# Performance work log

Hardware: AMD Instinct MI355X
Metric: run time of the kernel (lower is better)

Reference implementation:

```python
import jax, jax.numpy as jnp
import numpy as np

NL, ND, NM = 16384, 4096, 2048   # LncRNA / Disease / MiRNA node counts
E = 262144                       # edges per relation
FEAT, HID, OUTF = 256, 64, 128
ITEMS, SIZE = 4096, 2048


def setup_inputs() -> dict:
    key = jax.random.key(0)
    ks = jax.random.split(key, 32)
    f32 = jnp.float32

    def ed(i, n_src, n_dst):
        return (jax.random.randint(ks[i], (E,), 0, n_src),
                jax.random.randint(ks[i + 1], (E,), 0, n_dst))

    src_LD, dst_LD = ed(0, NL, ND)
    src_DL, dst_DL = ed(2, ND, NL)
    src_LM, dst_LM = ed(4, NL, NM)
    src_ML, dst_ML = ed(6, NM, NL)
    src_DM, dst_DM = ed(8, ND, NM)
    src_MD, dst_MD = ed(10, NM, ND)

    inp = dict(
        h_L=jax.random.normal(ks[12], (NL, FEAT), f32),
        h_D=jax.random.normal(ks[13], (ND, FEAT), f32),
        h_M=jax.random.normal(ks[14], (NM, FEAT), f32),
        Adj=jax.random.uniform(ks[15], (SIZE, ITEMS), f32),
        src_LD=src_LD, dst_LD=dst_LD, src_DL=src_DL, dst_DL=dst_DL,
        src_LM=src_LM, dst_LM=dst_LM, src_ML=src_ML, dst_ML=dst_ML,
        src_DM=src_DM, dst_DM=dst_DM, src_MD=src_MD, dst_MD=dst_MD,
        # GraphConv weights, stacked over the 6 relations in order
        # [LvsD, DvsL, LvsM, MvsL, DvsM, MvsD]
        W1=jax.random.normal(ks[16], (6, FEAT, HID), f32) * 0.05,
        b1=jnp.zeros((6, HID), f32),
        W2=jax.random.normal(ks[17], (6, HID, HID), f32) * 0.05,
        b2=jnp.zeros((6, HID), f32),
        W3=jax.random.normal(ks[18], (6, HID, OUTF), f32) * 0.05,
        b3=jnp.zeros((6, OUTF), f32),
        # dense MLP head
        f1_w=jax.random.normal(ks[19], (ITEMS + OUTF, 256), f32) * 0.02,
        f1_b=jnp.zeros((256,), f32),
        f2_w=jax.random.normal(ks[20], (256, 512), f32) * 0.05,
        f2_b=jnp.zeros((512,), f32),
        f3_w=jax.random.normal(ks[21], (512, 1024), f32) * 0.05,
        f3_b=jnp.zeros((1024,), f32),
        f4_w=jax.random.normal(ks[22], (1024, ITEMS), f32) * 0.03,
        f4_b=jnp.zeros((ITEMS,), f32),
        size=SIZE,
        leftIndex=0,
    )
    return inp


def _gconv(x, src, dst, n_dst, W, b):
    """DGL GraphConv with norm='both': D_dst^{-1/2} A D_src^{-1/2} X W + b.
    Degrees are clamped to >=1 (DGL behavior)."""
    n_src = x.shape[0]
    ones = jnp.ones(src.shape[0], x.dtype)
    out_deg = jnp.clip(jax.ops.segment_sum(ones, src, num_segments=n_src), 1.0)
    in_deg = jnp.clip(jax.ops.segment_sum(ones, dst, num_segments=n_dst), 1.0)
    feat = x * jax.lax.rsqrt(out_deg)[:, None]
    m = jax.ops.segment_sum(feat[src], dst, num_segments=n_dst)
    m = m * jax.lax.rsqrt(in_deg)[:, None]
    return m @ W + b


def reference(h_L, h_D, h_M, Adj,
              W1, b1, W2, b2, W3, b3,
              f1_w, f1_b, f2_w, f2_b, f3_w, f3_b, f4_w, f4_b,
              src_LD, dst_LD, src_DL, dst_DL, src_LM, dst_LM,
              src_ML, dst_ML, src_DM, dst_DM, src_MD, dst_MD,
              size, leftIndex):

    def hetero_layer(hL, hD, hM, W, b):
        # aggregate='sum' over edge types per destination node type
        oD = (_gconv(hL, src_LD, dst_LD, ND, W[0], b[0])
              + _gconv(hM, src_MD, dst_MD, ND, W[5], b[5]))
        oL = (_gconv(hD, src_DL, dst_DL, NL, W[1], b[1])
              + _gconv(hM, src_ML, dst_ML, NL, W[3], b[3]))
        oM = (_gconv(hL, src_LM, dst_LM, NM, W[2], b[2])
              + _gconv(hD, src_DM, dst_DM, NM, W[4], b[4]))
        return oL, oD, oM

    hL, hD, hM = hetero_layer(h_L, h_D, h_M, W1, b1)
    hL, hD, hM = hetero_layer(hL, hD, hM, W2, b2)
    hL, hD, hM = hetero_layer(hL, hD, hM, W3, b3)

    # F.normalize(p=1, dim=1): x / max(||x||_1, 1e-12)
    l1 = jnp.maximum(jnp.sum(jnp.abs(hL), axis=1, keepdims=True), 1e-12)
    lncrna = hL / l1

    fake_embedding = lncrna[leftIndex:leftIndex + size]  # [size, OUTF]
    x = jnp.concatenate([Adj, fake_embedding], axis=1)   # [size, ITEMS+OUTF]
    x = jax.nn.relu(x @ f1_w + f1_b)
    x = jax.nn.relu(x @ f2_w + f2_b)
    x = jax.nn.relu(x @ f3_w + f3_b)
    x = jax.nn.sigmoid(x @ f4_w + f4_b)
    return (fake_embedding, x)
```

## Files before the change

### kernel.cpp

```cpp
#include <hip/hip_runtime.h>

constexpr int kNL = 16384, kND = 4096, kNM = 2048;
constexpr int kE = 262144;
constexpr int kFEAT = 256, kHID = 64, kOUTF = 128;
constexpr int kITEMS = 4096, kSIZE = 2048;
constexpr int kHB = 16;
constexpr int kZS = 128;
constexpr int kXIN = kITEMS + kOUTF;

typedef unsigned short ushort_t;
typedef unsigned int uint_t;
typedef __attribute__((ext_vector_type(8))) short short8v;
typedef __attribute__((ext_vector_type(4))) float f32x4;
typedef __attribute__((ext_vector_type(4))) uint_t uint4v;
typedef __attribute__((ext_vector_type(2))) uint_t uint2v;
typedef __attribute__((ext_vector_type(4))) int int4v;

struct EdgePtrs { const int* p[12]; };
struct I6 { int v[6]; };

__device__ inline ushort_t f2bf(float f) {
  unsigned u = __builtin_bit_cast(unsigned, f);
  unsigned r = u + 0x7fffu + ((u >> 16) & 1u);
  return (ushort_t)(r >> 16);
}
__device__ inline float bf2f(ushort_t b) {
  unsigned u = ((unsigned)b) << 16;
  return __builtin_bit_cast(float, u);
}
__device__ inline float bf2f_lo(uint_t v) { return __builtin_bit_cast(float, v << 16); }
__device__ inline float bf2f_hi(uint_t v) { return __builtin_bit_cast(float, v & 0xffff0000u); }

__device__ __forceinline__ void gload16(const ushort_t* g, ushort_t* l) {
  __builtin_amdgcn_global_load_lds(
      (const __attribute__((address_space(1))) void*)g,
      (__attribute__((address_space(3))) void*)l, 16, 0, 0);
}

__device__ __forceinline__ void xcd_swizzle(int& bx, int& by) {
  int gx = gridDim.x, gy = gridDim.y;
  int nwg = gx * gy;
  int orig = by * gx + bx;
  int q = nwg >> 3, r = nwg & 7;
  int xcd = orig & 7, loc = orig >> 3;
  int s = ((xcd < r) ? xcd * (q + 1) : r * (q + 1) + (xcd - r) * q) + loc;
  by = s % gy;
  bx = s / gy;
}

__global__ __launch_bounds__(256) void hist_kernel(EdgePtrs ep, uint_t* __restrict__ part) {
  __shared__ uint_t bins[16384];
  int k = blockIdx.x >> 4, chunk = blockIdx.x & (kHB - 1);
  uint4v zero = {0, 0, 0, 0};
  for (int i = threadIdx.x; i < 4096; i += 256) ((uint4v*)bins)[i] = zero;
  __syncthreads();
  const int4v* arr = (const int4v*)(ep.p[k] + chunk * (kE / kHB));
  for (int i = threadIdx.x; i < kE / kHB / 4; i += 256) {
    int4v e4 = arr[i];
    atomicAdd(&bins[e4[0]], 1u);
    atomicAdd(&bins[e4[1]], 1u);
    atomicAdd(&bins[e4[2]], 1u);
    atomicAdd(&bins[e4[3]], 1u);
  }
  __syncthreads();
  uint4v* o = (uint4v*)(part + ((size_t)blockIdx.x << 14));
  for (int i = threadIdx.x; i < 4096; i += 256) o[i] = ((uint4v*)bins)[i];
}

struct PJob { const float* in; ushort_t* out; int A; int B; int C; int kind; int nblk; };
struct PJobs { PJob j[24]; int n; };

__global__ __launch_bounds__(256) void prep_kernel(PJobs jobs) {
  __shared__ float t64[64][65];
  int b = blockIdx.x;
  int ji = 0;
  while (ji < jobs.n && b >= jobs.j[ji].nblk) { b -= jobs.j[ji].nblk; ++ji; }
  if (ji >= jobs.n) return;
  PJob jb = jobs.j[ji];
  if (jb.kind == 0) {
    int idx = b * 256 + threadIdx.x;
    if (idx >= jb.A) return;
    float4 v = ((const float4*)jb.in)[idx];
    uint2v pk;
    pk[0] = (uint_t)f2bf(v.x) | ((uint_t)f2bf(v.y) << 16);
    pk[1] = (uint_t)f2bf(v.z) | ((uint_t)f2bf(v.w) << 16);
    *(uint2v*)(jb.out + (size_t)idx * 4) = pk;
  } else if (jb.kind == 2) {
    int idx = b * 256 + threadIdx.x;
    if (idx >= jb.A) return;
    float4 v = ((const float4*)jb.in)[idx];
    int row = idx >> jb.B, col4 = idx & ((1 << jb.B) - 1);
    uint2v pk;
    pk[0] = (uint_t)f2bf(v.x) | ((uint_t)f2bf(v.y) << 16);
    pk[1] = (uint_t)f2bf(v.z) | ((uint_t)f2bf(v.w) << 16);
    *(uint2v*)(jb.out + (size_t)row * jb.C + (size_t)col4 * 4) = pk;
  } else {
    int K = jb.A, N = jb.B;
    int tpr = N >> 6;
    int n0 = (b % tpr) * 64, k0 = (b / tpr) * 64;
    int tx = threadIdx.x & 15, ty = threadIdx.x >> 4;
#pragma unroll
    for (int i = 0; i < 64; i += 16) {
      float4 v = *(const float4*)(&jb.in[(size_t)(k0 + ty + i) * N + n0 + 4 * tx]);
      t64[ty + i][4 * tx + 0] = v.x;
      t64[ty + i][4 * tx + 1] = v.y;
      t64[ty + i][4 * tx + 2] = v.z;
      t64[ty + i][4 * tx + 3] = v.w;
    }
    __syncthreads();
#pragma unroll
    for (int i = 0; i < 64; i += 16) {
      int n = n0 + ty + i;
      float a0 = t64[4 * tx + 0][ty + i];
      float a1 = t64[4 * tx + 1][ty + i];
      float a2 = t64[4 * tx + 2][ty + i];
      float a3 = t64[4 * tx + 3][ty + i];
      uint2v pk;
      pk[0] = (uint_t)f2bf(a0) | ((uint_t)f2bf(a1) << 16);
      pk[1] = (uint_t)f2bf(a2) | ((uint_t)f2bf(a3) << 16);
      *(uint2v*)(&jb.out[(size_t)n * K + k0 + 4 * tx]) = pk;
    }
  }
}

__global__ void reduce_finalize_kernel(const uint_t* __restrict__ part,
                                       uint_t* __restrict__ cnts,
                                       float* __restrict__ degscale) {
  int idx = blockIdx.x * 256 + threadIdx.x;
  int k = idx >> 14, bin = idx & 16383;
  uint_t s = 0;
  for (int c = 0; c < kHB; ++c) s += part[((size_t)(k * kHB + c) << 14) + bin];
  cnts[idx] = s;
  degscale[idx] = rsqrtf((float)max(s, 1u));
}

__global__ __launch_bounds__(1024) void scan_kernel(const uint_t* __restrict__ cnts,
                                                    uint_t* __restrict__ rp_all,
                                                    I6 rpoff, I6 nd) {
  __shared__ uint_t sums[1024];
  int t = blockIdx.x;
  int n = nd.v[t];
  const uint_t* c = cnts + ((size_t)(2 * t + 1) << 14);
  uint_t* rp = rp_all + rpoff.v[t];
  int tid = threadIdx.x;
  int seg = n >> 10;
  uint_t s = 0;
  for (int j = 0; j < seg; ++j) s += c[tid * seg + j];
  sums[tid] = s;
  __syncthreads();
  for (int o = 1; o < 1024; o <<= 1) {
    uint_t v = (tid >= o) ? sums[tid - o] : 0u;
    __syncthreads();
    sums[tid] += v;
    __syncthreads();
  }
  uint_t run = sums[tid] - s;
  for (int j = 0; j < seg; ++j) { rp[tid * seg + j] = run; run += c[tid * seg + j]; }
  if (tid == 1023) rp[n] = run;
}

__global__ void chunkofs_kernel(const uint_t* __restrict__ part,
                                const uint_t* __restrict__ rp_all,
                                I6 rpoff, I6 nd, uint_t* __restrict__ ofs) {
  int idx = blockIdx.x * 256 + threadIdx.x;
  int t = idx >> 14, bin = idx & 16383;
  if (bin >= nd.v[t]) return;
  uint_t run = (rp_all + rpoff.v[t])[bin];
  for (int c = 0; c < kHB; ++c) {
    ofs[((size_t)(t * kHB + c) << 14) + bin] = run;
    run += part[((size_t)((2 * t + 1) * kHB + c) << 14) + bin];
  }
}

__global__ __launch_bounds__(256) void fill_kernel(EdgePtrs ep,
                                                   const uint_t* __restrict__ ofs,
                                                   ushort_t* __restrict__ csr_all) {
  __shared__ uint_t cursor[16384];
  int t = blockIdx.x >> 4, chunk = blockIdx.x & (kHB - 1);
  const uint_t* o = ofs + ((size_t)(t * kHB + chunk) << 14);
  for (int i = threadIdx.x; i < 16384; i += 256) cursor[i] = o[i];
  __syncthreads();
  int base = chunk * (kE / kHB);
  const int4v* srcp = (const int4v*)(ep.p[2 * t] + base);
  const int4v* dstp = (const int4v*)(ep.p[2 * t + 1] + base);
  ushort_t* csr = csr_all + (size_t)t * kE;
  for (int i = threadIdx.x; i < kE / kHB / 4; i += 256) {
    int4v d4 = dstp[i];
    int4v s4 = srcp[i];
#pragma unroll
    for (int j = 0; j < 4; ++j) {
      uint_t pos = atomicAdd(&cursor[d4[j]], 1u);
      csr[pos] = (ushort_t)s4[j];
    }
  }
}

__global__ __launch_bounds__(256) void gemm_bf16_kernel(
    const ushort_t* __restrict__ A, const ushort_t* __restrict__ Bt,
    const float* __restrict__ Cin, void* __restrict__ out, int outBf16,
    int M, int N, int K, int ldb,
    const float* __restrict__ bias, int act,
    int kChunk, float* __restrict__ partOut) {
  __shared__ ushort_t As[2][8192];
  __shared__ ushort_t Bs[2][8192];
  int tid = threadIdx.x;
  int wave = tid >> 6, lane = tid & 63;
  int bx = blockIdx.x, by = blockIdx.y;
  xcd_swizzle(bx, by);
  int brow = by * 128, bcol = bx * 128;
  int kStart = partOut ? blockIdx.z * kChunk : 0;
  int kLen = partOut ? kChunk : K;
  int nsteps = kLen >> 6;

  int rowBase = tid >> 3;
  int u = (tid & 7) ^ (rowBase & 7);
  const ushort_t* gA = A + (size_t)(brow + rowBase) * K + kStart + u * 8;
  const ushort_t* gB = Bt + (size_t)(bcol + rowBase) * ldb + kStart + u * 8;

  int fr = lane & 15, fq = lane >> 4;
  f32x4 acc[2][8] = {};

#define STAGE_G(buf, koff)                                              \
  do {                                                                  \
    _Pragma("unroll")                                                   \
    for (int j = 0; j < 4; ++j) {                                       \
      gload16(gA + (size_t)j * 32 * K + (koff), &As[buf][j * 2048 + tid * 8]);   \
      gload16(gB + (size_t)j * 32 * ldb + (koff), &Bs[buf][j * 2048 + tid * 8]); \
    }                                                                   \
  } while (0)

  STAGE_G(0, 0);
  int cur = 0;
  for (int i = 0; i < nsteps; ++i) {
    __syncthreads();
    if (i + 1 < nsteps) STAGE_G(cur ^ 1, (i + 1) * 64);
#pragma unroll
    for (int kk = 0; kk < 2; ++kk) {
      short8v af[2], bfr[8];
#pragma unroll
      for (int mi = 0; mi < 2; ++mi) {
        int row = wave * 32 + mi * 16 + fr;
        af[mi] = *(const short8v*)(&As[cur][row * 64 + (((kk * 4 + fq) ^ (row & 7)) * 8)]);
      }
#pragma unroll
      for (int ni = 0; ni < 8; ++ni) {
        int row = ni * 16 + fr;
        bfr[ni] = *(const short8v*)(&Bs[cur][row * 64 + (((kk * 4 + fq) ^ (row & 7)) * 8)]);
      }
#pragma unroll
      for (int mi = 0; mi < 2; ++mi)
#pragma unroll
        for (int ni = 0; ni < 8; ++ni)
          acc[mi][ni] = __builtin_amdgcn_mfma_f32_16x16x32_bf16(af[mi], bfr[ni], acc[mi][ni], 0, 0, 0);
    }
    cur ^= 1;
  }
#undef STAGE_G

  if (partOut) {
    float* o = partOut + (size_t)blockIdx.z * M * N;
#pragma unroll
    for (int mi = 0; mi < 2; ++mi)
#pragma unroll
      for (int ni = 0; ni < 8; ++ni)
#pragma unroll
        for (int r = 0; r < 4; ++r) {
          int row = brow + wave * 32 + mi * 16 + fq * 4 + r;
          int col = bcol + ni * 16 + fr;
          o[(size_t)row * N + col] = acc[mi][ni][r];
        }
    return;
  }
#pragma unroll
  for (int mi = 0; mi < 2; ++mi)
#pragma unroll
    for (int ni = 0; ni < 8; ++ni)
#pragma unroll
      for (int r = 0; r < 4; ++r) {
        int row = brow + wave * 32 + mi * 16 + fq * 4 + r;
        int col = bcol + ni * 16 + fr;
        float v = acc[mi][ni][r];
        if (Cin) v += Cin[(size_t)row * N + col];
        if (bias) v += bias[col];
        if (act == 1) v = fmaxf(v, 0.0f);
        else if (act == 2) v = 1.0f / (1.0f + expf(-v));
        if (outBf16) ((ushort_t*)out)[(size_t)row * N + col] = f2bf(v);
        else ((float*)out)[(size_t)row * N + col] = v;
      }
}

__global__ __launch_bounds__(512) void gemm256_kernel(
    const ushort_t* __restrict__ A, const ushort_t* __restrict__ Bt,
    float* __restrict__ out, int M, int N, int K,
    const float* __restrict__ bias) {
  __shared__ ushort_t As[3][16384];
  __shared__ ushort_t Bs[3][8192];
  int tid = threadIdx.x;
  int wave = tid >> 6, lane = tid & 63;
  int bx = blockIdx.x, by = blockIdx.y;
  if (gridDim.x == 32 && gridDim.y == 8) {
    int o = by * 32 + bx;
    int X = o & 7, loc = o >> 3;
    bx = (X & 3) * 8 + (loc & 7);
    by = (X >> 2) * 4 + (loc >> 3);
  } else {
    xcd_swizzle(bx, by);
  }
  int fr = lane & 15, fq = lane >> 4;
  int wm = wave >> 2, wn = wave & 3;

  int rquot = tid >> 3;
  int uslot = (tid & 7) ^ (rquot & 7);
  const ushort_t* gA = A + (size_t)(by * 256 + rquot) * K + uslot * 8;
  const ushort_t* gB = Bt + (size_t)(bx * 128 + rquot) * K + uslot * 8;

  f32x4 acc[8][2] = {};
  int nsteps = K >> 6;

#define SG_A(b_, t_, j_) gload16(gA + (size_t)(j_) * 64 * K + (size_t)(t_) * 64, &As[b_][(j_) * 4096 + tid * 8])
#define SG_B(b_, t_, j_) gload16(gB + (size_t)(j_) * 64 * K + (size_t)(t_) * 64, &Bs[b_][(j_) * 4096 + tid * 8])

  SG_A(0, 0, 0); SG_A(0, 0, 1); SG_A(0, 0, 2); SG_A(0, 0, 3); SG_B(0, 0, 0); SG_B(0, 0, 1);
  SG_A(1, 1, 0); SG_A(1, 1, 1); SG_A(1, 1, 2); SG_A(1, 1, 3); SG_B(1, 1, 0); SG_B(1, 1, 1);
  asm volatile("s_waitcnt vmcnt(6)" ::: "memory");
  __builtin_amdgcn_s_barrier();

  short8v bf[2][2];

#define PHASE(p_)                                                            \
  {                                                                          \
    short8v af[4][2];                                                        \
    _Pragma("unroll")                                                        \
    for (int q = 0; q < 4; ++q) {                                            \
      int row = wm * 128 + (4 * (p_) + q) * 16 + fr;                         \
      int base = row * 64;                                                   \
      af[q][0] = *(const short8v*)(&As[b][base + ((fq ^ (row & 7)) * 8)]);   \
      af[q][1] = *(const short8v*)(&As[b][base + (((4 + fq) ^ (row & 7)) * 8)]); \
    }                                                                        \
    if ((p_) == 0) {                                                         \
      _Pragma("unroll")                                                      \
      for (int q = 0; q < 2; ++q) {                                          \
        int row = wn * 32 + q * 16 + fr;                                     \
        int base = row * 64;                                                 \
        bf[q][0] = *(const short8v*)(&Bs[b][base + ((fq ^ (row & 7)) * 8)]); \
        bf[q][1] = *(const short8v*)(&Bs[b][base + (((4 + fq) ^ (row & 7)) * 8)]); \
      }                                                                      \
      if (doStage) { SG_A(sb, t + 2, 0); SG_A(sb, t + 2, 1); SG_A(sb, t + 2, 2); SG_A(sb, t + 2, 3); } \
    } else {                                                                 \
      if (doStage) { SG_B(sb, t + 2, 0); SG_B(sb, t + 2, 1); }               \
      if (t + 2 < nsteps)      asm volatile("s_waitcnt vmcnt(6)" ::: "memory"); \
      else if (t + 1 < nsteps) asm volatile("s_waitcnt vmcnt(0)" ::: "memory"); \
    }                                                                        \
    __builtin_amdgcn_s_barrier();                                            \
    asm volatile("s_waitcnt lgkmcnt(0)" ::: "memory");                       \
    __builtin_amdgcn_s_setprio(1);                                           \
    _Pragma("unroll")                                                        \
    for (int kk = 0; kk < 2; ++kk)                                           \
      _Pragma("unroll")                                                      \
      for (int q = 0; q < 4; ++q)                                            \
        _Pragma("unroll")                                                    \
        for (int ni = 0; ni < 2; ++ni)                                       \
          acc[4 * (p_) + q][ni] = __builtin_amdgcn_mfma_f32_16x16x32_bf16(af[q][kk], bf[ni][kk], acc[4 * (p_) + q][ni], 0, 0, 0); \
    __builtin_amdgcn_s_setprio(0);                                           \
    __builtin_amdgcn_s_barrier();                                            \
  }

  for (int t = 0; t < nsteps; ++t) {
    int b = t % 3, sb = (t + 2) % 3;
    bool doStage = (t + 2 < nsteps);
    PHASE(0);
    PHASE(1);
  }
#undef PHASE
#undef SG_A
#undef SG_B

#pragma unroll
  for (int mi = 0; mi < 8; ++mi)
#pragma unroll
    for (int ni = 0; ni < 2; ++ni)
#pragma unroll
      for (int r = 0; r < 4; ++r) {
        int row = by * 256 + wm * 128 + mi * 16 + fq * 4 + r;
        int col = bx * 128 + wn * 32 + ni * 16 + fr;
        float v = acc[mi][ni][r] + bias[col];
        out[(size_t)row * N + col] = 1.0f / (1.0f + expf(-v));
      }
}

struct ZDesc { const ushort_t* A; const ushort_t* Bt; ushort_t* out;
               const float* rs0; const float* rs1; int M; int K; };
struct ZDescs { ZDesc d[3]; };

__global__ __launch_bounds__(256) void zgemm_batched_kernel(ZDescs ds) {
  __shared__ ushort_t As[2][8192];
  __shared__ ushort_t Bs[2][8192];
  ZDesc de = ds.d[blockIdx.z];
  int gy = gridDim.y;
  int yq = gy >> 3;
  int ys = (blockIdx.y & 7) * yq + (blockIdx.y >> 3);
  int brow = ys * 128;
  if (brow >= de.M) return;
  int K = de.K;
  int nsteps = K >> 6;
  if (nsteps == 0) nsteps = 1;
  int kkMax = (K >= 64) ? 2 : 1;
  int tid = threadIdx.x;
  int wave = tid >> 6, lane = tid & 63;

  int rowBase = tid >> 3;
  int u = (tid & 7) ^ (rowBase & 7);
  const ushort_t* gA = de.A + (size_t)(brow + rowBase) * K + u * 8;
  const ushort_t* gB = de.Bt + (size_t)rowBase * K + u * 8;

  int fr = lane & 15, fq = lane >> 4;
  f32x4 acc[2][8] = {};

#define STAGE_Z(buf, koff)                                              \
  do {                                                                  \
    _Pragma("unroll")                                                   \
    for (int j = 0; j < 4; ++j) {                                       \
      gload16(gA + (size_t)j * 32 * K + (koff), &As[buf][j * 2048 + tid * 8]); \
      gload16(gB + (size_t)j * 32 * K + (koff), &Bs[buf][j * 2048 + tid * 8]); \
    }                                                                   \
  } while (0)

  STAGE_Z(0, 0);
  int cur = 0;
  for (int i = 0; i < nsteps; ++i) {
    __syncthreads();
    if (i + 1 < nsteps) STAGE_Z(cur ^ 1, (i + 1) * 64);
#pragma unroll
    for (int kk = 0; kk < 2; ++kk) {
      if (kk >= kkMax) break;
      short8v af[2], bfr[8];
#pragma unroll
      for (int mi = 0; mi < 2; ++mi) {
        int row = wave * 32 + mi * 16 + fr;
        af[mi] = *(const short8v*)(&As[cur][row * 64 + (((kk * 4 + fq) ^ (row & 7)) * 8)]);
      }
#pragma unroll
      for (int ni = 0; ni < 8; ++ni) {
        int row = ni * 16 + fr;
        bfr[ni] = *(const short8v*)(&Bs[cur][row * 64 + (((kk * 4 + fq) ^ (row & 7)) * 8)]);
      }
#pragma unroll
      for (int mi = 0; mi < 2; ++mi)
#pragma unroll
        for (int ni = 0; ni < 8; ++ni)
          acc[mi][ni] = __builtin_amdgcn_mfma_f32_16x16x32_bf16(af[mi], bfr[ni], acc[mi][ni], 0, 0, 0);
    }
    cur ^= 1;
  }
#undef STAGE_Z

#pragma unroll
  for (int mi = 0; mi < 2; ++mi)
#pragma unroll
    for (int ni = 0; ni < 8; ++ni) {
      const float* rs = (ni < 4) ? de.rs0 : de.rs1;
#pragma unroll
      for (int r = 0; r < 4; ++r) {
        int row = brow + wave * 32 + mi * 16 + fq * 4 + r;
        int col = ni * 16 + fr;
        de.out[(size_t)row * 128 + col] = f2bf(acc[mi][ni][r] * rs[row]);
      }
    }
}

struct GDesc { const ushort_t* z0; const uint_t* rp0; const ushort_t* cs0; const float* s0;
               const ushort_t* z1; const uint_t* rp1; const ushort_t* cs1; const float* s1;
               const float* b0; const float* b1; ushort_t* out; int nd; };
struct GDescs { GDesc d[3]; };

__device__ __forceinline__ void acc8(float* __restrict__ a, uint4v v) {
  a[0] += bf2f_lo(v[0]); a[1] += bf2f_hi(v[0]);
  a[2] += bf2f_lo(v[1]); a[3] += bf2f_hi(v[1]);
  a[4] += bf2f_lo(v[2]); a[5] += bf2f_hi(v[2]);
  a[6] += bf2f_lo(v[3]); a[7] += bf2f_hi(v[3]);
}

__device__ __forceinline__ void gsum64(const ushort_t* __restrict__ z,
                                       const ushort_t* __restrict__ cs,
                                       uint_t e, uint_t ee, int h, int off,
                                       float* __restrict__ a) {
  for (; e + 16 <= ee; e += 16) {
    uint_t sA = cs[e + h], sB = cs[e + 8 + h];
    uint4v vA = *(const uint4v*)(z + (size_t)sA * kZS + off);
    uint4v vB = *(const uint4v*)(z + (size_t)sB * kZS + off);
    acc8(a, vA); acc8(a, vB);
  }
  for (; e + 8 <= ee; e += 8) {
    uint4v v = *(const uint4v*)(z + (size_t)cs[e + h] * kZS + off);
    acc8(a, v);
  }
  if ((uint_t)h < ee - e) {
    uint4v v = *(const uint4v*)(z + (size_t)cs[e + h] * kZS + off);
    acc8(a, v);
  }
}

__global__ __launch_bounds__(256) void gather_batched_kernel(GDescs ds) {
  GDesc de = ds.d[blockIdx.z];
  int d = blockIdx.x * 4 + (threadIdx.x >> 6);
  if (d >= de.nd) return;
  int lane = threadIdx.x & 63;
  int h = lane >> 3, c = lane & 7;
  int off = 8 * c;
  float a0[8] = {}, a1[8] = {};
  gsum64(de.z0, de.cs0, de.rp0[d], de.rp0[d + 1], h, off, a0);
  gsum64(de.z1, de.cs1, de.rp1[d], de.rp1[d + 1], h, off, a1);
  float s0 = de.s0[d], s1 = de.s1[d];
  float v[8];
#pragma unroll
  for (int j = 0; j < 8; ++j) {
    v[j] = a0[j] * s0 + a1[j] * s1;
    v[j] += __shfl_xor(v[j], 8);
    v[j] += __shfl_xor(v[j], 16);
    v[j] += __shfl_xor(v[j], 32);
  }
  if (h == 0) {
    int c0 = off;
    uint4v pack;
#pragma unroll
    for (int j = 0; j < 4; ++j) {
      float x = v[2 * j] + de.b0[c0 + 2 * j] + de.b1[c0 + 2 * j];
      float y = v[2 * j + 1] + de.b0[c0 + 2 * j + 1] + de.b1[c0 + 2 * j + 1];
      pack[j] = (uint_t)f2bf(x) | ((uint_t)f2bf(y) << 16);
    }
    *(uint4v*)(de.out + (size_t)d * 64 + c0) = pack;
  }
}

__device__ __forceinline__ void gsum128(const ushort_t* __restrict__ z,
                                        const ushort_t* __restrict__ cs,
                                        uint_t e, uint_t ee, int h, int off,
                                        float* __restrict__ a) {
  for (; e + 8 <= ee; e += 8) {
    uint_t sA = cs[e + h], sB = cs[e + 4 + h];
    uint4v vA = *(const uint4v*)(z + (size_t)sA * 128 + off);
    uint4v vB = *(const uint4v*)(z + (size_t)sB * 128 + off);
    acc8(a, vA); acc8(a, vB);
  }
  for (; e + 4 <= ee; e += 4) {
    uint4v v = *(const uint4v*)(z + (size_t)cs[e + h] * 128 + off);
    acc8(a, v);
  }
  if ((uint_t)h < ee - e) {
    uint4v v = *(const uint4v*)(z + (size_t)cs[e + h] * 128 + off);
    acc8(a, v);
  }
}

__global__ __launch_bounds__(256) void gather128_l1_kernel(
    const ushort_t* __restrict__ zD, const uint_t* __restrict__ rpD, const ushort_t* __restrict__ csD,
    const float* __restrict__ sInD,
    const ushort_t* __restrict__ zM, const uint_t* __restrict__ rpM, const ushort_t* __restrict__ csM,
    const float* __restrict__ sInM,
    const float* __restrict__ bD, const float* __restrict__ bM,
    float* __restrict__ emb, ushort_t* __restrict__ embb, int embStride) {
  int d = blockIdx.x * 4 + (threadIdx.x >> 6);
  int lane = threadIdx.x & 63;
  int h = lane >> 4, c = lane & 15;
  int off = 8 * c;
  float aD[8] = {}, aM[8] = {};
  gsum128(zD, csD, rpD[d], rpD[d + 1], h, off, aD);
  gsum128(zM, csM, rpM[d], rpM[d + 1], h, off, aM);
  float sD = sInD[d], sM = sInM[d];
  float v[8];
#pragma unroll
  for (int j = 0; j < 8; ++j) {
    v[j] = aD[j] * sD + aM[j] * sM + bD[off + j] + bM[off + j];
    v[j] += __shfl_xor(v[j], 16);
    v[j] += __shfl_xor(v[j], 32);
  }
  float a = 0;
#pragma unroll
  for (int j = 0; j < 8; ++j) a += fabsf(v[j]);
#pragma unroll
  for (int o = 8; o > 0; o >>= 1) a += __shfl_xor(a, o);
  float l1 = fmaxf(a, 1e-12f);
  if (h == 0) {
    float e0[8];
#pragma unroll
    for (int j = 0; j < 8; ++j) e0[j] = v[j] / l1;
    float* ep_ = emb + (size_t)d * kOUTF + off;
    *(f32x4*)ep_ = {e0[0], e0[1], e0[2], e0[3]};
    *(f32x4*)(ep_ + 4) = {e0[4], e0[5], e0[6], e0[7]};
    uint4v pack;
#pragma unroll
    for (int j = 0; j < 4; ++j)
      pack[j] = (uint_t)f2bf(e0[2 * j]) | ((uint_t)f2bf(e0[2 * j + 1]) << 16);
    *(uint4v*)(embb + (size_t)d * embStride + off) = pack;
  }
}

__global__ void reducek_kernel(const float* __restrict__ P, void* __restrict__ out,
                               int outBf16, int n4, int S, int N,
                               const float* __restrict__ bias, int act) {
  int idx = blockIdx.x * 256 + threadIdx.x;
  if (idx >= n4) return;
  float4 a = ((const float4*)P)[idx];
  for (int s = 1; s < S; ++s) {
    float4 b = ((const float4*)P)[(size_t)s * n4 + idx];
    a.x += b.x; a.y += b.y; a.z += b.z; a.w += b.w;
  }
  float v[4] = {a.x, a.y, a.z, a.w};
  int c0 = (idx * 4) % N;
#pragma unroll
  for (int j = 0; j < 4; ++j) {
    if (bias) v[j] += bias[c0 + j];
    if (act == 1) v[j] = fmaxf(v[j], 0.0f);
    else if (act == 2) v[j] = 1.0f / (1.0f + expf(-v[j]));
  }
  if (outBf16) {
    ushort_t* o = (ushort_t*)out + (size_t)idx * 4;
    o[0] = f2bf(v[0]); o[1] = f2bf(v[1]); o[2] = f2bf(v[2]); o[3] = f2bf(v[3]);
  } else {
    float4 r = {v[0], v[1], v[2], v[3]};
    ((float4*)out)[idx] = r;
  }
}

extern "C" void kernel_launch(void* const* d_in, const int* in_sizes, int n_in,
                              void* d_out, int out_size, void* d_ws, size_t ws_size,
                              hipStream_t stream) {
  const float* h_L = (const float*)d_in[0];
  const float* h_D = (const float*)d_in[1];
  const float* h_M = (const float*)d_in[2];
  const float* Adj = (const float*)d_in[3];
  EdgePtrs ep;
  for (int i = 0; i < 12; ++i) ep.p[i] = (const int*)d_in[4 + i];
  const float* W[3]  = {(const float*)d_in[16], (const float*)d_in[18], (const float*)d_in[20]};
  const float* Bb[3] = {(const float*)d_in[17], (const float*)d_in[19], (const float*)d_in[21]};
  const float* f1_w = (const float*)d_in[22];
  const float* f1_b = (const float*)d_in[23];
  const float* f2_w = (const float*)d_in[24];
  const float* f2_b = (const float*)d_in[25];
  const float* f3_w = (const float*)d_in[26];
  const float* f3_b = (const float*)d_in[27];
  const float* f4_w = (const float*)d_in[28];
  const float* f4_b = (const float*)d_in[29];

  float* ws = (float*)d_ws;
  size_t off = 0;
  auto allocF = [&](size_t n) { float* p = ws + off; off += (n + 3) & ~(size_t)3; return p; };
  auto allocU = [&](size_t n) { return (uint_t*)allocF(n); };
  auto allocB = [&](size_t n) { return (ushort_t*)allocF((n + 1) / 2); };

  uint_t* part   = allocU((size_t)12 * kHB * 16384);
  uint_t* cnts   = allocU((size_t)12 * 16384);
  float*  degscale = allocF((size_t)12 * 16384);
  uint_t* rp_all = allocU(45062 + 2);
  uint_t* ofs    = allocU((size_t)6 * kHB * 16384);
  ushort_t* csr  = allocB((size_t)6 * kE);
  ushort_t* hLb  = allocB((size_t)kNL * kFEAT);
  ushort_t* hDb  = allocB((size_t)kND * kFEAT);
  ushort_t* hMb  = allocB((size_t)kNM * kFEAT);
  ushort_t* xin  = allocB((size_t)kSIZE * kXIN);
  ushort_t* aLb  = allocB((size_t)kNL * kHID);
  ushort_t* aDb  = allocB((size_t)kND * kHID);
  ushort_t* aMb  = allocB((size_t)kNM * kHID);
  ushort_t* WLt  = allocB((size_t)128 * kFEAT);
  ushort_t* WDt  = allocB((size_t)128 * kFEAT);
  ushort_t* WMt  = allocB((size_t)128 * kFEAT);
  ushort_t* WL2t = allocB((size_t)128 * kHID);
  ushort_t* WD2t = allocB((size_t)128 * kHID);
  ushort_t* WM2t = allocB((size_t)128 * kHID);
  ushort_t* W3t1 = allocB((size_t)kOUTF * kHID);
  ushort_t* W3t3 = allocB((size_t)kOUTF * kHID);
  ushort_t* f1t  = allocB((size_t)256 * kXIN);
  ushort_t* f2t  = allocB((size_t)512 * 256);
  ushort_t* f3t  = allocB((size_t)1024 * 512);
  ushort_t* f4t  = allocB((size_t)kITEMS * 1024);
  ushort_t* x1b  = allocB((size_t)kSIZE * 256);
  ushort_t* x2b  = allocB((size_t)kSIZE * 512);
  ushort_t* x3b  = allocB((size_t)kSIZE * 1024);

  int S1 = 1, S2 = 1, S3 = 1;
  float* partK = nullptr;
  size_t avail = (ws_size / 4 > off) ? ws_size / 4 - off - 64 : 0;
  size_t needBig = (size_t)11 * kSIZE * 256;
  size_t needStd = (size_t)4 * kSIZE * 512;
  if (avail >= needBig + 16) {
    partK = allocF(needBig);
    S1 = 11; S2 = 4; S3 = 2;
  } else if (avail >= needStd + 16) {
    partK = allocF(needStd);
    S1 = 6; S2 = 4; S3 = 2;
  }

  ushort_t* zL  = (ushort_t*)part;
  ushort_t* zD  = zL + (size_t)kNL * kZS;
  ushort_t* zM  = zD + (size_t)kND * kZS;
  ushort_t* zD3 = zM + (size_t)kNM * kZS;
  ushort_t* zM3 = zD3 + (size_t)kND * kZS;

  I6 ndI; const int ndst_[6] = {kND, kNL, kNM, kNL, kNM, kND};
  for (int t = 0; t < 6; ++t) ndI.v[t] = ndst_[t];
  I6 rpo; { int r = 0; for (int t = 0; t < 6; ++t) { rpo.v[t] = r; r += ndst_[t] + 1; } }
  auto dsc = [&](int k) { return degscale + ((size_t)k << 14); };

  hist_kernel<<<12 * kHB, 256, 0, stream>>>(ep, part);

  PJobs pj; int nj = 0; int totblk = 0;
  auto addCvt = [&](const float* in, ushort_t* out, size_t n) {
    int n4 = (int)(n / 4);
    pj.j[nj] = {in, out, n4, 0, 0, 0, (n4 + 255) / 256}; totblk += pj.j[nj].nblk; ++nj;
  };
  auto addStrided = [&](const float* in, ushort_t* out, size_t n, int log2RowLen4, int stride) {
    int n4 = (int)(n / 4);
    pj.j[nj] = {in, out, n4, log2RowLen4, stride, 2, (n4 + 255) / 256}; totblk += pj.j[nj].nblk; ++nj;
  };
  auto addT = [&](const float* in, ushort_t* out, int K, int N) {
    pj.j[nj] = {in, out, K, N, 0, 1, (N / 64) * (K / 64)}; totblk += pj.j[nj].nblk; ++nj;
  };
  addCvt(h_L, hLb, (size_t)kNL * kFEAT);
  addCvt(h_D, hDb, (size_t)kND * kFEAT);
  addCvt(h_M, hMb, (size_t)kNM * kFEAT);
  addStrided(Adj, xin, (size_t)kSIZE * kITEMS, 10, kXIN);
  addT(W[0] + (size_t)0 * kFEAT * kHID, WLt + (size_t)0 * kFEAT, kFEAT, kHID);
  addT(W[0] + (size_t)2 * kFEAT * kHID, WLt + (size_t)64 * kFEAT, kFEAT, kHID);
  addT(W[0] + (size_t)1 * kFEAT * kHID, WDt + (size_t)0 * kFEAT, kFEAT, kHID);
  addT(W[0] + (size_t)4 * kFEAT * kHID, WDt + (size_t)64 * kFEAT, kFEAT, kHID);
  addT(W[0] + (size_t)3 * kFEAT * kHID, WMt + (size_t)0 * kFEAT, kFEAT, kHID);
  addT(W[0] + (size_t)5 * kFEAT * kHID, WMt + (size_t)64 * kFEAT, kFEAT, kHID);
  addT(W[1] + (size_t)0 * kHID * kHID, WL2t + (size_t)0 * kHID, kHID, kHID);
  addT(W[1] + (size_t)2 * kHID * kHID, WL2t + (size_t)64 * kHID, kHID, kHID);
  addT(W[1] + (size_t)1 * kHID * kHID, WD2t + (size_t)0 * kHID, kHID, kHID);
  addT(W[1] + (size_t)4 * kHID * kHID, WD2t + (size_t)64 * kHID, kHID, kHID);
  addT(W[1] + (size_t)3 * kHID * kHID, WM2t + (size_t)0 * kHID, kHID, kHID);
  addT(W[1] + (size_t)5 * kHID * kHID, WM2t + (size_t)64 * kHID, kHID, kHID);
  addT(W[2] + (size_t)1 * kHID * kOUTF, W3t1, kHID, kOUTF);
  addT(W[2] + (size_t)3 * kHID * kOUTF, W3t3, kHID, kOUTF);
  addT(f1_w, f1t, kXIN, 256);
  addT(f2_w, f2t, 256, 512);
  addT(f3_w, f3t, 512, 1024);
  addT(f4_w, f4t, 1024, kITEMS);
  pj.n = nj;
  prep_kernel<<<totblk, 256, 0, stream>>>(pj);

  reduce_finalize_kernel<<<12 * 16384 / 256, 256, 0, stream>>>(part, cnts, degscale);
  scan_kernel<<<6, 1024, 0, stream>>>(cnts, rp_all, rpo, ndI);
  chunkofs_kernel<<<6 * 16384 / 256, 256, 0, stream>>>(part, rp_all, rpo, ndI, ofs);
  fill_kernel<<<6 * kHB, 256, 0, stream>>>(ep, ofs, csr);

  const ushort_t* curb[3] = {hLb, hDb, hMb};
  for (int layer = 0; layer < 2; ++layer) {
    int K = (layer == 0) ? kFEAT : kHID;
    const ushort_t* WtL = (layer == 0) ? WLt : WL2t;
    const ushort_t* WtD = (layer == 0) ? WDt : WD2t;
    const ushort_t* WtM = (layer == 0) ? WMt : WM2t;
    const float* bl = Bb[layer];
    ZDescs zd;
    zd.d[0] = {curb[0], WtL, zL, dsc(0), dsc(4),  kNL, K};
    zd.d[1] = {curb[1], WtD, zD, dsc(2), dsc(8),  kND, K};
    zd.d[2] = {curb[2], WtM, zM, dsc(6), dsc(10), kNM, K};
    zgemm_batched_kernel<<<dim3(1, kNL / 128, 3), 256, 0, stream>>>(zd);
    if (layer == 0) {
      GDescs gd;
      gd.d[0] = {zD, rp_all + rpo.v[1], csr + (size_t)1 * kE, dsc(3),
                 zM, rp_all + rpo.v[3], csr + (size_t)3 * kE, dsc(7),
                 bl + 1 * kHID, bl + 3 * kHID, aLb, kNL};
      gd.d[1] = {zL, rp_all + rpo.v[0], csr + (size_t)0 * kE, dsc(1),
                 zM + 64, rp_all + rpo.v[5], csr + (size_t)5 * kE, dsc(11),
                 bl + 0 * kHID, bl + 5 * kHID, aDb, kND};
      gd.d[2] = {zL + 64, rp_all + rpo.v[2], csr + (size_t)2 * kE, dsc(5),
                 zD + 64, rp_all + rpo.v[4], csr + (size_t)4 * kE, dsc(9),
                 bl + 2 * kHID, bl + 4 * kHID, aMb, kNM};
      gather_batched_kernel<<<dim3(kNL / 4, 1, 3), 256, 0, stream>>>(gd);
    } else {
      GDescs gd;
      gd.d[0] = {zL, rp_all + rpo.v[0], csr + (size_t)0 * kE, dsc(1),
                 zM + 64, rp_all + rpo.v[5], csr + (size_t)5 * kE, dsc(11),
                 bl + 0 * kHID, bl + 5 * kHID, aDb, kND};
      gd.d[1] = {zL + 64, rp_all + rpo.v[2], csr + (size_t)2 * kE, dsc(5),
                 zD + 64, rp_all + rpo.v[4], csr + (size_t)4 * kE, dsc(9),
                 bl + 2 * kHID, bl + 4 * kHID, aMb, kNM};
      gd.d[2] = gd.d[1];
      gather_batched_kernel<<<dim3(kND / 4, 1, 2), 256, 0, stream>>>(gd);
    }
    curb[0] = aLb; curb[1] = aDb; curb[2] = aMb;
  }

  float* emb  = (float*)d_out;
  float* outx = (float*)d_out + (size_t)kSIZE * kOUTF;
  {
    ZDescs zd;
    zd.d[0] = {curb[1], W3t1, zD3, dsc(2), dsc(2), kND, kHID};
    zd.d[1] = {curb[2], W3t3, zM3, dsc(6), dsc(6), kNM, kHID};
    zd.d[2] = zd.d[1];
    zgemm_batched_kernel<<<dim3(1, kND / 128, 2), 256, 0, stream>>>(zd);
    gather128_l1_kernel<<<kSIZE / 4, 256, 0, stream>>>(
        zD3, rp_all + rpo.v[1], csr + (size_t)1 * kE, dsc(3),
        zM3, rp_all + rpo.v[3], csr + (size_t)3 * kE, dsc(7),
        Bb[2] + 1 * kOUTF, Bb[2] + 3 * kOUTF, emb, xin + kITEMS, kXIN);
  }

  if (S1 > 1) {
    gemm_bf16_kernel<<<dim3(2, 16, S1), 256, 0, stream>>>(
        xin, f1t, nullptr, nullptr, 0, kSIZE, 256, kXIN, kXIN,
        nullptr, 0, kXIN / S1, partK);
    int n4 = kSIZE * 256 / 4;
    reducek_kernel<<<(n4 + 255) / 256, 256, 0, stream>>>(
        partK, x1b, 1, n4, S1, 256, f1_b, 1);
  } else {
    gemm_bf16_kernel<<<dim3(2, 16, 1), 256, 0, stream>>>(
        xin, f1t, nullptr, x1b, 1, kSIZE, 256, kXIN, kXIN, f1_b, 1, 0, nullptr);
  }
  if (S2 > 1) {
    gemm_bf16_kernel<<<dim3(4, 16, S2), 256, 0, stream>>>(
        x1b, f2t, nullptr, nullptr, 0, kSIZE, 512, 256, 256,
        nullptr, 0, 256 / S2, partK);
    int n4 = kSIZE * 512 / 4;
    reducek_kernel<<<(n4 + 255) / 256, 256, 0, stream>>>(
        partK, x2b, 1, n4, S2, 512, f2_b, 1);
  } else {
    gemm_bf16_kernel<<<dim3(4, 16, 1), 256, 0, stream>>>(
        x1b, f2t, nullptr, x2b, 1, kSIZE, 512, 256, 256, f2_b, 1, 0, nullptr);
  }
  if (S3 > 1) {
    gemm_bf16_kernel<<<dim3(8, 16, S3), 256, 0, stream>>>(
        x2b, f3t, nullptr, nullptr, 0, kSIZE, 1024, 512, 512,
        nullptr, 0, 512 / S3, partK);
    int n4 = kSIZE * 1024 / 4;
    reducek_kernel<<<(n4 + 255) / 256, 256, 0, stream>>>(
        partK, x3b, 1, n4, S3, 1024, f3_b, 1);
  } else {
    gemm_bf16_kernel<<<dim3(8, 16, 1), 256, 0, stream>>>(
        x2b, f3t, nullptr, x3b, 1, kSIZE, 1024, 512, 512, f3_b, 1, 0, nullptr);
  }
  gemm256_kernel<<<dim3(kITEMS / 128, kSIZE / 256), 512, 0, stream>>>(
      x3b, f4t, outx, kSIZE, kITEMS, 1024, f4_b);
}
```

Measured before the change: 250.2 us.

## Fuse next-layer Z projection into gather kernel, dropping separate zgemm launches

The gather kernel now stages the next layer's transposed weight in swizzled LDS. After aggregating each destination row, it multiplies the row by that weight inside the same wave and writes the scaled Z output directly. This removes the layer-2 and layer-3 zgemm launches and the intermediate bf16 activation round trips through global memory. The cost is an 8K-element weight load into LDS in every block, and the per-wave dot products run on scalar FP32 FMAs instead of MFMA. Z buffers are reallocated to hold separate layer outputs, with zD3/zM3 aliased onto zL.

```diff
diff --git a/kernel.cpp b/kernel.cpp
--- a/kernel.cpp
+++ b/kernel.cpp
@@ -468,11 +468,6 @@
     }
 }
 
-struct GDesc { const ushort_t* z0; const uint_t* rp0; const ushort_t* cs0; const float* s0;
-               const ushort_t* z1; const uint_t* rp1; const ushort_t* cs1; const float* s1;
-               const float* b0; const float* b1; ushort_t* out; int nd; };
-struct GDescs { GDesc d[3]; };
-
 __device__ __forceinline__ void acc8(float* __restrict__ a, uint4v v) {
   a[0] += bf2f_lo(v[0]); a[1] += bf2f_hi(v[0]);
   a[2] += bf2f_lo(v[1]); a[3] += bf2f_hi(v[1]);
@@ -500,11 +495,28 @@
   }
 }
 
-__global__ __launch_bounds__(256) void gather_batched_kernel(GDescs ds) {
-  GDesc de = ds.d[blockIdx.z];
-  int d = blockIdx.x * 4 + (threadIdx.x >> 6);
+struct GZDesc { const ushort_t* z0; const uint_t* rp0; const ushort_t* cs0; const float* s0;
+                const ushort_t* z1; const uint_t* rp1; const ushort_t* cs1; const float* s1;
+                const float* b0; const float* b1;
+                const ushort_t* Wt; const float* ro0; const float* ro1;
+                ushort_t* zout; int nd; };
+struct GZDescs { GZDesc d[3]; };
+
+__global__ __launch_bounds__(256) void gatherz_kernel(GZDescs ds) {
+  __shared__ ushort_t Wl[8192];
+  __shared__ ushort_t abuf[4][64];
+  GZDesc de = ds.d[blockIdx.z];
+  int tid = threadIdx.x;
+  for (int i = tid; i < 1024; i += 256) {
+    int col = i >> 3, kk = i & 7;
+    uint4v w = *(const uint4v*)(de.Wt + (size_t)i * 8);
+    *(uint4v*)(&Wl[col * 64 + ((kk ^ (col & 7)) << 3)]) = w;
+  }
+  __syncthreads();
+  int wv = tid >> 6;
+  int d = blockIdx.x * 4 + wv;
   if (d >= de.nd) return;
-  int lane = threadIdx.x & 63;
+  int lane = tid & 63;
   int h = lane >> 3, c = lane & 7;
   int off = 8 * c;
   float a0[8] = {}, a1[8] = {};
@@ -518,18 +530,30 @@
     v[j] += __shfl_xor(v[j], 8);
     v[j] += __shfl_xor(v[j], 16);
     v[j] += __shfl_xor(v[j], 32);
-  }
-  if (h == 0) {
-    int c0 = off;
-    uint4v pack;
-#pragma unroll
-    for (int j = 0; j < 4; ++j) {
-      float x = v[2 * j] + de.b0[c0 + 2 * j] + de.b1[c0 + 2 * j];
-      float y = v[2 * j + 1] + de.b0[c0 + 2 * j + 1] + de.b1[c0 + 2 * j + 1];
-      pack[j] = (uint_t)f2bf(x) | ((uint_t)f2bf(y) << 16);
+    v[j] += de.b0[off + j] + de.b1[off + j];
+  }
+  uint4v apack;
+#pragma unroll
+  for (int j = 0; j < 4; ++j)
+    apack[j] = (uint_t)f2bf(v[2 * j]) | ((uint_t)f2bf(v[2 * j + 1]) << 16);
+  if (h == 0) *(uint4v*)(&abuf[wv][off]) = apack;
+  asm volatile("s_waitcnt lgkmcnt(0)" ::: "memory");
+  float acc0 = 0.0f, acc1 = 0.0f;
+  int sw = lane & 7;
+#pragma unroll
+  for (int kk = 0; kk < 8; ++kk) {
+    uint4v av = *(const uint4v*)(&abuf[wv][kk * 8]);
+    uint4v w0 = *(const uint4v*)(&Wl[lane * 64 + ((kk ^ sw) << 3)]);
+    uint4v w1 = *(const uint4v*)(&Wl[(lane + 64) * 64 + ((kk ^ sw) << 3)]);
+#pragma unroll
+    for (int u = 0; u < 4; ++u) {
+      float alo = bf2f_lo(av[u]), ahi = bf2f_hi(av[u]);
+      acc0 += alo * bf2f_lo(w0[u]) + ahi * bf2f_hi(w0[u]);
+      acc1 += alo * bf2f_lo(w1[u]) + ahi * bf2f_hi(w1[u]);
     }
-    *(uint4v*)(de.out + (size_t)d * 64 + c0) = pack;
-  }
+  }
+  de.zout[(size_t)d * 128 + lane]      = f2bf(acc0 * de.ro0[d]);
+  de.zout[(size_t)d * 128 + 64 + lane] = f2bf(acc1 * de.ro1[d]);
 }
 
 __device__ __forceinline__ void gsum128(const ushort_t* __restrict__ z,
@@ -658,9 +682,6 @@
   ushort_t* hDb  = allocB((size_t)kND * kFEAT);
   ushort_t* hMb  = allocB((size_t)kNM * kFEAT);
   ushort_t* xin  = allocB((size_t)kSIZE * kXIN);
-  ushort_t* aLb  = allocB((size_t)kNL * kHID);
-  ushort_t* aDb  = allocB((size_t)kND * kHID);
-  ushort_t* aMb  = allocB((size_t)kNM * kHID);
   ushort_t* WLt  = allocB((size_t)128 * kFEAT);
   ushort_t* WDt  = allocB((size_t)128 * kFEAT);
   ushort_t* WMt  = allocB((size_t)128 * kFEAT);
@@ -693,8 +714,11 @@
   ushort_t* zL  = (ushort_t*)part;
   ushort_t* zD  = zL + (size_t)kNL * kZS;
   ushort_t* zM  = zD + (size_t)kND * kZS;
-  ushort_t* zD3 = zM + (size_t)kNM * kZS;
-  ushort_t* zM3 = zD3 + (size_t)kND * kZS;
+  ushort_t* zL2 = zM + (size_t)kNM * kZS;
+  ushort_t* zD2 = zL2 + (size_t)kNL * kZS;
+  ushort_t* zM2 = zD2 + (size_t)kND * kZS;
+  ushort_t* zD3 = zL;
+  ushort_t* zM3 = zL + (size_t)kND * kZS;
 
   I6 ndI; const int ndst_[6] = {kND, kNL, kNM, kNL, kNM, kND};
   for (int t = 0; t < 6; ++t) ndI.v[t] = ndst_[t];
@@ -745,57 +769,49 @@
   chunkofs_kernel<<<6 * 16384 / 256, 256, 0, stream>>>(part, rp_all, rpo, ndI, ofs);
   fill_kernel<<<6 * kHB, 256, 0, stream>>>(ep, ofs, csr);
 
-  const ushort_t* curb[3] = {hLb, hDb, hMb};
-  for (int layer = 0; layer < 2; ++layer) {
-    int K = (layer == 0) ? kFEAT : kHID;
-    const ushort_t* WtL = (layer == 0) ? WLt : WL2t;
-    const ushort_t* WtD = (layer == 0) ? WDt : WD2t;
-    const ushort_t* WtM = (layer == 0) ? WMt : WM2t;
-    const float* bl = Bb[layer];
+  {
     ZDescs zd;
-    zd.d[0] = {curb[0], WtL, zL, dsc(0), dsc(4),  kNL, K};
-    zd.d[1] = {curb[1], WtD, zD, dsc(2), dsc(8),  kND, K};
-    zd.d[2] = {curb[2], WtM, zM, dsc(6), dsc(10), kNM, K};
+    zd.d[0] = {hLb, WLt, zL, dsc(0), dsc(4),  kNL, kFEAT};
+    zd.d[1] = {hDb, WDt, zD, dsc(2), dsc(8),  kND, kFEAT};
+    zd.d[2] = {hMb, WMt, zM, dsc(6), dsc(10), kNM, kFEAT};
     zgemm_batched_kernel<<<dim3(1, kNL / 128, 3), 256, 0, stream>>>(zd);
-    if (layer == 0) {
-      GDescs gd;
-      gd.d[0] = {zD, rp_all + rpo.v[1], csr + (size_t)1 * kE, dsc(3),
-                 zM, rp_all + rpo.v[3], csr + (size_t)3 * kE, dsc(7),
-                 bl + 1 * kHID, bl + 3 * kHID, aLb, kNL};
-      gd.d[1] = {zL, rp_all + rpo.v[0], csr + (size_t)0 * kE, dsc(1),
-                 zM + 64, rp_all + rpo.v[5], csr + (size_t)5 * kE, dsc(11),
-                 bl + 0 * kHID, bl + 5 * kHID, aDb, kND};
-      gd.d[2] = {zL + 64, rp_all + rpo.v[2], csr + (size_t)2 * kE, dsc(5),
-                 zD + 64, rp_all + rpo.v[4], csr + (size_t)4 * kE, dsc(9),
-                 bl + 2 * kHID, bl + 4 * kHID, aMb, kNM};
-      gather_batched_kernel<<<dim3(kNL / 4, 1, 3), 256, 0, stream>>>(gd);
-    } else {
-      GDescs gd;
-      gd.d[0] = {zL, rp_all + rpo.v[0], csr + (size_t)0 * kE, dsc(1),
-                 zM + 64, rp_all + rpo.v[5], csr + (size_t)5 * kE, dsc(11),
-                 bl + 0 * kHID, bl + 5 * kHID, aDb, kND};
-      gd.d[1] = {zL + 64, rp_all + rpo.v[2], csr + (size_t)2 * kE, dsc(5),
-                 zD + 64, rp_all + rpo.v[4], csr + (size_t)4 * kE, dsc(9),
-                 bl + 2 * kHID, bl + 4 * kHID, aMb, kNM};
-      gd.d[2] = gd.d[1];
-      gather_batched_kernel<<<dim3(kND / 4, 1, 2), 256, 0, stream>>>(gd);
-    }
-    curb[0] = aLb; curb[1] = aDb; curb[2] = aMb;
+  }
+  {
+    GZDescs gz;
+    gz.d[0] = {zD, rp_all + rpo.v[1], csr + (size_t)1 * kE, dsc(3),
+               zM, rp_all + rpo.v[3], csr + (size_t)3 * kE, dsc(7),
+               Bb[0] + 1 * kHID, Bb[0] + 3 * kHID,
+               WL2t, dsc(0), dsc(4), zL2, kNL};
+    gz.d[1] = {zL, rp_all + rpo.v[0], csr + (size_t)0 * kE, dsc(1),
+               zM + 64, rp_all + rpo.v[5], csr + (size_t)5 * kE, dsc(11),
+               Bb[0] + 0 * kHID, Bb[0] + 5 * kHID,
+               WD2t, dsc(2), dsc(8), zD2, kND};
+    gz.d[2] = {zL + 64, rp_all + rpo.v[2], csr + (size_t)2 * kE, dsc(5),
+               zD + 64, rp_all + rpo.v[4], csr + (size_t)4 * kE, dsc(9),
+               Bb[0] + 2 * kHID, Bb[0] + 4 * kHID,
+               WM2t, dsc(6), dsc(10), zM2, kNM};
+    gatherz_kernel<<<dim3(kNL / 4, 1, 3), 256, 0, stream>>>(gz);
+  }
+  {
+    GZDescs gz;
+    gz.d[0] = {zL2, rp_all + rpo.v[0], csr + (size_t)0 * kE, dsc(1),
+               zM2 + 64, rp_all + rpo.v[5], csr + (size_t)5 * kE, dsc(11),
+               Bb[1] + 0 * kHID, Bb[1] + 5 * kHID,
+               W3t1, dsc(2), dsc(2), zD3, kND};
+    gz.d[1] = {zL2 + 64, rp_all + rpo.v[2], csr + (size_t)2 * kE, dsc(5),
+               zD2 + 64, rp_all + rpo.v[4], csr + (size_t)4 * kE, dsc(9),
+               Bb[1] + 2 * kHID, Bb[1] + 4 * kHID,
+               W3t3, dsc(6), dsc(6), zM3, kNM};
+    gz.d[2] = gz.d[1];
+    gatherz_kernel<<<dim3(kND / 4, 1, 2), 256, 0, stream>>>(gz);
   }
 
   float* emb  = (float*)d_out;
   float* outx = (float*)d_out + (size_t)kSIZE * kOUTF;
-  {
-    ZDescs zd;
-    zd.d[0] = {curb[1], W3t1, zD3, dsc(2), dsc(2), kND, kHID};
-    zd.d[1] = {curb[2], W3t3, zM3, dsc(6), dsc(6), kNM, kHID};
-    zd.d[2] = zd.d[1];
-    zgemm_batched_kernel<<<dim3(1, kND / 128, 2), 256, 0, stream>>>(zd);
-    gather128_l1_kernel<<<kSIZE / 4, 256, 0, stream>>>(
-        zD3, rp_all + rpo.v[1], csr + (size_t)1 * kE, dsc(3),
-        zM3, rp_all + rpo.v[3], csr + (size_t)3 * kE, dsc(7),
-        Bb[2] + 1 * kOUTF, Bb[2] + 3 * kOUTF, emb, xin + kITEMS, kXIN);
-  }
+  gather128_l1_kernel<<<kSIZE / 4, 256, 0, stream>>>(
+      zD3, rp_all + rpo.v[1], csr + (size_t)1 * kE, dsc(3),
+      zM3, rp_all + rpo.v[3], csr + (size_t)3 * kE, dsc(7),
+      Bb[2] + 1 * kOUTF, Bb[2] + 3 * kOUTF, emb, xin + kITEMS, kXIN);
 
   if (S1 > 1) {
     gemm_bf16_kernel<<<dim3(2, 16, S1), 256, 0, stream>>>(
```

New measurement: 255.0 us. No clear change (+1.9%).
